# Kernel tuning notes

Measured on AMD Instinct MI355X. Metric: run time of the kernel, lower is better.

Reference implementation:

```python
import jax, jax.numpy as jnp
import numpy as np

STRIDE = 4
NUM_HEADS = 8


def _make_window(x, stride, nh):
    # (B,C,H,W) -> (B, nh, S, S, (H/S)*(W/S), C/nh)
    b, c, h, w = x.shape
    x = x.reshape(b, nh, c // nh, h // stride, stride, w // stride, stride)
    x = x.transpose(0, 1, 4, 6, 3, 5, 2)
    return x.reshape(b, nh, stride, stride, (h // stride) * (w // stride), c // nh)


def _demake_window(x, h, w):
    # (B, nh, S, S, L, dh) -> (B, nh*dh, H, W)
    b, nh, s, _, L, dh = x.shape
    x = x.reshape(b, nh, s, s, h // s, w // s, dh)
    x = x.transpose(0, 1, 6, 4, 2, 5, 3)
    return x.reshape(b, nh * dh, h, w)


def _proj(x, W, bias):
    # 1x1 conv == per-pixel GEMM: (B,C,H,W),(O,C) -> (B,O,H,W)
    return jnp.einsum('bchw,oc->bohw', x, W) + bias[None, :, None, None]


def setup_inputs() -> dict:
    key = jax.random.key(0)
    ks = jax.random.split(key, 12)
    B, C, H, W = 4, 256, 64, 64
    P, V, O = 256, 256, 256  # proj/value/out channels
    inp = {
        'fea_q': jax.random.normal(ks[0], (B, C, H, W), jnp.float32),
        'fea_k': jax.random.normal(ks[1], (B, C, H, W), jnp.float32),
        'fea_v': jax.random.normal(ks[2], (B, V, H, W), jnp.float32),
        'mask_q': (jax.random.uniform(ks[3], (B, 1, H, W)) > 0.5).astype(jnp.float32),
        'mask_k': (jax.random.uniform(ks[4], (B, 1, H, W)) > 0.5).astype(jnp.float32),
        'q_w': jax.random.normal(ks[5], (P, C), jnp.float32) * 0.02,
        'q_b': jnp.zeros((P,), jnp.float32),
        'k_w': jax.random.normal(ks[6], (P, C), jnp.float32) * 0.02,
        'k_b': jnp.zeros((P,), jnp.float32),
        'v_w': jax.random.normal(ks[7], (O, V), jnp.float32) * 0.02,
        'v_b': jnp.zeros((O,), jnp.float32),
    }
    return inp


def reference(fea_q, fea_k, fea_v, mask_q, mask_k, q_w, q_b, k_w, k_b, v_w, v_b):
    B, _, H, W = fea_q.shape
    head_dim = q_w.shape[0] // NUM_HEADS
    scaling = head_dim ** (-0.5)

    query = _make_window(_proj(fea_q, q_w, q_b), STRIDE, NUM_HEADS)
    key = _make_window(_proj(fea_k, k_w, k_b), STRIDE, NUM_HEADS)
    value = _make_window(_proj(fea_v, v_w, v_b), STRIDE, NUM_HEADS)

    # (B, nh, S, S, L, L)
    weights = jnp.matmul(query, jnp.swapaxes(key, -1, -2)) * scaling

    # mask attention (no-grad in original)
    mq = _make_window(jax.lax.stop_gradient(mask_q), STRIDE, 1)
    mk = _make_window(jax.lax.stop_gradient(mask_k), STRIDE, 1)
    mask_attn = jnp.matmul(mq, jnp.swapaxes(mk, -1, -2))  # (B,1,S,S,L,L)
    mask_sum = jnp.sum(mask_attn, axis=-1, keepdims=True)
    mask_attn = mask_attn + (mask_sum == 0).astype(jnp.float32)
    mask_attn = jnp.where(mask_attn == 0, -jnp.inf,
                          jnp.where(mask_attn == 1, 0.0, mask_attn))
    weights = weights + mask_attn

    weights = jax.nn.softmax(weights, axis=-1)  # dropout p=0 -> identity
    weights = weights * (1.0 - (mask_sum == 0).astype(jnp.float32))

    out = jnp.matmul(weights, value)  # (B, nh, S, S, L, dh)
    return _demake_window(out, H, W)
```

## Files before the change

### kernel.cpp

```cpp
#include <hip/hip_runtime.h>
#include <hip/hip_bf16.h>

#define NH 8
#define DH 32
#define LW 256
#define HW 4096
#define CIN 256

typedef float f32x4 __attribute__((ext_vector_type(4)));
typedef short s16x8 __attribute__((ext_vector_type(8)));
typedef short s16x4 __attribute__((ext_vector_type(4)));

#define AS1 __attribute__((address_space(1)))
#define AS3 __attribute__((address_space(3)))

__device__ __forceinline__ short f2bf(float f) {
  __hip_bfloat16 h = __float2bfloat16(f);
  short s; __builtin_memcpy(&s, &h, 2); return s;
}

__device__ __forceinline__ void gload_lds16(const void* g, void* l) {
  __builtin_amdgcn_global_load_lds((const AS1 void*)g, (AS3 void*)l, 16, 0, 0);
}

#define KOFF 4194304
#define VOFF 8388608
#define WTOFF 12582912

__global__ void wconv_kernel(const float* __restrict__ qw, const float* __restrict__ kw,
                             const float* __restrict__ vw, short* __restrict__ ws) {
  int blk = blockIdx.x;
  int t = blk >> 5, kb = blk & 31;
  const float* W = (t == 0) ? qw : ((t == 1) ? kw : vw);
  int o = threadIdx.x;
  f32x4 w0 = *(const f32x4*)(W + o * CIN + kb * 8);
  f32x4 w1 = *(const f32x4*)(W + o * CIN + kb * 8 + 4);
  s16x8 v;
#pragma unroll
  for (int j = 0; j < 4; ++j) { v[j] = f2bf(w0[j]); v[4 + j] = f2bf(w1[j]); }
  *(s16x8*)(ws + WTOFF + (blk * 256 + o) * 8) = v;
}

__global__ void __launch_bounds__(256, 3)
proj_kernel(const float* __restrict__ fq, const float* __restrict__ fk,
            const float* __restrict__ fv,
            const float* __restrict__ qb, const float* __restrict__ kb_,
            const float* __restrict__ vb,
            short* __restrict__ ws) {
  __shared__ s16x8 SMEM[2112];

  int bid = blockIdx.x;
  int orig = (bid & 7) * 96 + (bid >> 3);
  int t = orig >> 8;
  int r0 = orig & 255;
  int b = r0 >> 6;
  int pblk = r0 & 63;

  const float* fea = (t == 0) ? fq : ((t == 1) ? fk : fv);
  const float* Bv  = (t == 0) ? qb : ((t == 1) ? kb_ : vb);
  const short* Wt  = ws + WTOFF + t * 65536;

  int p0 = pblk * 64;
  int tid = threadIdx.x;
  int lane = tid & 63, wv = tid >> 6;
  int g = lane >> 4, li = lane & 15;

  const f32x4 fzero = {0.f, 0.f, 0.f, 0.f};
  f32x4 acc[4][4];
#pragma unroll
  for (int m = 0; m < 4; ++m)
#pragma unroll
    for (int n = 0; n < 4; ++n) acc[m][n] = fzero;

  const float* feab = fea + b * (CIN * HW);
  int wq = tid & 15;
  int jh = (tid >> 4) & 1;
  int coct = tid >> 5;

  f32x4 ldB[4];

#define LOAD_B(cs_) do { int c0_ = (cs_) * 64; _Pragma("unroll") \
  for (int j_ = 0; j_ < 4; ++j_) \
    ldB[j_] = *(const f32x4*)(feab + (c0_ + coct * 8 + jh * 4 + j_) * HW + p0 + wq * 4); } while (0)

#define WRITE_B(buf_) do { _Pragma("unroll") \
  for (int pp_ = 0; pp_ < 4; ++pp_) { s16x4 v_; _Pragma("unroll") \
    for (int j_ = 0; j_ < 4; ++j_) v_[j_] = f2bf(ldB[j_][pp_]); \
    int w_ = wq * 4 + pp_; int wsw_ = w_ ^ ((w_ >> 3) & 7); \
    *(s16x4*)((short*)SMEM + ((buf_) * 512 + coct * 64 + wsw_) * 8 + jh * 4) = v_; } } while (0)

  LOAD_B(0);
  WRITE_B(0);
  __syncthreads();

#pragma unroll
  for (int cs = 0; cs < 4; ++cs) {
    if (cs < 3) LOAD_B(cs + 1);
    s16x8 aF[2][4];
#pragma unroll
    for (int kk = 0; kk < 2; ++kk)
#pragma unroll
      for (int m = 0; m < 4; ++m)
        aF[kk][m] = *(const s16x8*)(Wt + ((cs * 8 + kk * 4 + g) * 256 + wv * 64 + m * 16 + li) * 8);
#pragma unroll
    for (int kk = 0; kk < 2; ++kk) {
#pragma unroll
      for (int n = 0; n < 4; ++n) {
        int w = n * 16 + li;
        int wsw = w ^ ((w >> 3) & 7);
        s16x8 bb = SMEM[(cs & 1) * 512 + (kk * 4 + g) * 64 + wsw];
#pragma unroll
        for (int m = 0; m < 4; ++m)
          acc[m][n] = __builtin_amdgcn_mfma_f32_16x16x32_bf16(aF[kk][m], bb, acc[m][n], 0, 0, 0);
      }
    }
    if (cs < 3) {
      WRITE_B((cs + 1) & 1);
      __syncthreads();
    }
  }
#undef LOAD_B
#undef WRITE_B

  float bias_r[4][4];
#pragma unroll
  for (int m = 0; m < 4; ++m) {
    f32x4 b4 = *(const f32x4*)(Bv + wv * 64 + m * 16 + g * 4);
#pragma unroll
    for (int rr = 0; rr < 4; ++rr) bias_r[m][rr] = b4[rr];
  }

  __syncthreads();
  short* Tr = (short*)SMEM;
#pragma unroll
  for (int m = 0; m < 4; ++m) {
    int ob = wv * 64 + m * 16 + g * 4;
#pragma unroll
    for (int n = 0; n < 4; ++n) {
      int w = n * 16 + li;
      s16x4 v;
#pragma unroll
      for (int rr = 0; rr < 4; ++rr) v[rr] = f2bf(acc[m][n][rr] + bias_r[m][rr]);
      *(s16x4*)(Tr + w * 264 + ob) = v;
    }
  }
  __syncthreads();

  int s1 = pblk & 3, h0 = pblk >> 2;
  if (t != 2) {
    short* dst = ws + (t == 0 ? 0 : KOFF);
#pragma unroll
    for (int it = 0; it < 8; ++it) {
      int o_oct = it * 4 + (tid >> 6);
      int w = tid & 63;
      s16x8 v = *(const s16x8*)(Tr + w * 264 + o_oct * 8);
      int o = o_oct * 8;
      int nh = o >> 5, kb = (o & 31) >> 3;
      int s2 = w & 3, w0 = w >> 2;
      int l = h0 * 16 + w0;
      int winbase = (b * NH + nh) * 16 + s1 * 4 + s2;
      *(s16x8*)(dst + winbase * 8192 + (kb * 256 + l) * 8) = v;
    }
  } else {
#pragma unroll
    for (int it = 0; it < 8; ++it) {
      int d = tid;
      int s2 = it & 3, w0h = it >> 2;
      int l_oct = h0 * 2 + w0h;
      s16x8 v;
#pragma unroll
      for (int k = 0; k < 8; ++k) {
        int w = (w0h * 8 + k) * 4 + s2;
        v[k] = Tr[w * 264 + d];
      }
      int dh = d & 31;
      int nh2 = d >> 5;
      int winbase = (b * NH + nh2) * 16 + s1 * 4 + s2;
      int idx = l_oct * 256 + (dh >> 4) * 128 + (dh & 15) * 8;
      *(s16x8*)(ws + VOFF + winbase * 8192 + idx) = v;
    }
  }
}

__global__ void __launch_bounds__(512, 4)
attn_kernel(const short* __restrict__ ws, const float* __restrict__ mq,
            const float* __restrict__ mk, float* __restrict__ out) {
  __shared__ s16x8 KsV[1024];
  __shared__ s16x8 PsV[1024];
  __shared__ float amaskS[256];
  __shared__ float mqS[256];
  __shared__ float facS[256];
  __shared__ int anyS[4];

  int bid = blockIdx.x;
  int orig = (bid & 7) * 64 + (bid >> 3);
  int s2 = orig & 3, s1 = (orig >> 2) & 3, nh = (orig >> 4) & 7, b = orig >> 7;
  int wwin = s1 * 4 + s2;
  int tid = threadIdx.x;
  int lane = tid & 63, wv = tid >> 6, g = lane >> 4, li = lane & 15;

  int winbase = (b * NH + nh) * 16 + wwin;
  const short* qt = ws + winbase * 8192;
  const short* kt = ws + KOFF + winbase * 8192;
  const short* vt = ws + VOFF + winbase * 8192;

#pragma unroll
  for (int i = 0; i < 2; ++i) {
    int seg = i * 8 + wv;
    gload_lds16(kt + (seg * 64 + lane) * 8, &KsV[seg * 64]);
  }

  if (tid < 256) {
    int l = tid;
    int h = (l >> 4) * 4 + s1, w = (l & 15) * 4 + s2;
    float mkv = mk[b * HW + h * 64 + w];
    amaskS[l] = (mkv > 0.5f) ? 0.0f : -1e30f;
    unsigned long long bal = __ballot(mkv > 0.5f);
    if (lane == 0) anyS[wv] = (bal != 0ULL) ? 1 : 0;
    mqS[l] = mq[b * HW + h * 64 + w];
  }

  int lq0 = wv * 32;
  s16x8 qa[2];
#pragma unroll
  for (int m = 0; m < 2; ++m)
    qa[m] = *(const s16x8*)(qt + (g * 256 + lq0 + m * 16 + li) * 8);

  __syncthreads();
  int anyk = anyS[0] | anyS[1] | anyS[2] | anyS[3];

  const f32x4 fzero = {0.f, 0.f, 0.f, 0.f};
  f32x4 of[2][2];
#pragma unroll
  for (int m = 0; m < 2; ++m) { of[m][0] = fzero; of[m][1] = fzero; }
  float rs[8];
#pragma unroll
  for (int i = 0; i < 8; ++i) rs[i] = 0.0f;

  const float C = 0.17677669529663689f * 1.4426950408889634f;

#pragma unroll
  for (int lkb = 0; lkb < 4; ++lkb) {
    f32x4 sa[2][4];
#pragma unroll
    for (int n = 0; n < 4; ++n) {
      s16x8 kf = KsV[g * 256 + lkb * 64 + n * 16 + li];
#pragma unroll
      for (int m = 0; m < 2; ++m)
        sa[m][n] = __builtin_amdgcn_mfma_f32_16x16x32_bf16(qa[m], kf, fzero, 0, 0, 0);
    }
#pragma unroll
    for (int ks = 0; ks < 2; ++ks) {
#pragma unroll
      for (int n2 = 0; n2 < 2; ++n2) {
        int n = ks * 2 + n2;
        float am = amaskS[lkb * 64 + n * 16 + li];
#pragma unroll
        for (int m = 0; m < 2; ++m) {
#pragma unroll
          for (int rr = 0; rr < 4; ++rr) {
            float pval = exp2f(sa[m][n][rr] * C + am);
            rs[m * 4 + rr] += pval;
            int row = m * 16 + g * 4 + rr;
            int cl = n * 16 + li;
            int kbh = (cl >> 3) & 3;
            short* ps = (short*)&PsV[wv * 128 + kbh * 32 + row];
            ps[cl & 7] = f2bf(pval);
          }
        }
      }
      int kg = lkb * 2 + ks;
      s16x8 pb[2];
#pragma unroll
      for (int n = 0; n < 2; ++n) pb[n] = PsV[wv * 128 + g * 32 + n * 16 + li];
#pragma unroll
      for (int m2 = 0; m2 < 2; ++m2) {
        s16x8 va = *(const s16x8*)(vt + (kg * 4 + g) * 256 + m2 * 128 + li * 8);
#pragma unroll
        for (int n = 0; n < 2; ++n)
          of[m2][n] = __builtin_amdgcn_mfma_f32_16x16x32_bf16(va, pb[n], of[m2][n], 0, 0, 0);
      }
    }
  }

#pragma unroll
  for (int i = 0; i < 8; ++i) {
    float v = rs[i];
    v += __shfl_xor(v, 1);
    v += __shfl_xor(v, 2);
    v += __shfl_xor(v, 4);
    v += __shfl_xor(v, 8);
    rs[i] = v;
  }
  if (li == 0) {
#pragma unroll
    for (int m = 0; m < 2; ++m)
#pragma unroll
      for (int rr = 0; rr < 4; ++rr) {
        int row = m * 16 + g * 4 + rr;
        float sum = rs[m * 4 + rr];
        facS[wv * 32 + row] = (anyk && mqS[wv * 32 + row] > 0.5f) ? (1.0f / sum) : 0.0f;
      }
  }

#pragma unroll
  for (int m2 = 0; m2 < 2; ++m2) {
#pragma unroll
    for (int n = 0; n < 2; ++n) {
      int l = wv * 32 + n * 16;
      float fac = facS[l + li];
      int h = (l >> 4) * 4 + s1;
      int w = li * 4 + s2;
#pragma unroll
      for (int rr = 0; rr < 4; ++rr) {
        int o = nh * 32 + m2 * 16 + g * 4 + rr;
        out[((b * 256 + o) * 64 + h) * 64 + w] = of[m2][n][rr] * fac;
      }
    }
  }
}

extern "C" void kernel_launch(void* const* d_in, const int* in_sizes, int n_in,
                              void* d_out, int out_size, void* d_ws, size_t ws_size,
                              hipStream_t stream) {
  const float* fq = (const float*)d_in[0];
  const float* fk = (const float*)d_in[1];
  const float* fv = (const float*)d_in[2];
  const float* mq = (const float*)d_in[3];
  const float* mk = (const float*)d_in[4];
  const float* qw = (const float*)d_in[5];
  const float* qb = (const float*)d_in[6];
  const float* kw = (const float*)d_in[7];
  const float* kb = (const float*)d_in[8];
  const float* vw = (const float*)d_in[9];
  const float* vb = (const float*)d_in[10];
  short* ws = (short*)d_ws;

  wconv_kernel<<<96, 256, 0, stream>>>(qw, kw, vw, ws);
  proj_kernel<<<768, 256, 0, stream>>>(fq, fk, fv, qb, kb, vb, ws);
  attn_kernel<<<512, 512, 0, stream>>>(ws, mq, mk, (float*)d_out);
}
```

Measured before the change: 48.71 us.

## Fuse projection and windowed attention into one kernel per window-head

Merges the separate projection kernel and attention kernel into one kernel in which each block projects the Q, K and V tiles for its own (batch, window, head) directly into LDS and then runs attention on them. This removes the bf16 Q/K/V round trip through global memory and one kernel launch. In exchange, each block re-reads the full 256-channel input features for its window's pixels with strided scalar fp32 loads, and those loads are repeated across the 8 heads. Block size also drops from 512 to 256 threads, with each wave handling more rows.

```diff
diff --git a/kernel.cpp b/kernel.cpp
--- a/kernel.cpp
+++ b/kernel.cpp
@@ -3,29 +3,17 @@
 
 #define NH 8
 #define DH 32
-#define LW 256
 #define HW 4096
 #define CIN 256
 
 typedef float f32x4 __attribute__((ext_vector_type(4)));
 typedef short s16x8 __attribute__((ext_vector_type(8)));
-typedef short s16x4 __attribute__((ext_vector_type(4)));
-
-#define AS1 __attribute__((address_space(1)))
-#define AS3 __attribute__((address_space(3)))
 
 __device__ __forceinline__ short f2bf(float f) {
   __hip_bfloat16 h = __float2bfloat16(f);
   short s; __builtin_memcpy(&s, &h, 2); return s;
 }
 
-__device__ __forceinline__ void gload_lds16(const void* g, void* l) {
-  __builtin_amdgcn_global_load_lds((const AS1 void*)g, (AS3 void*)l, 16, 0, 0);
-}
-
-#define KOFF 4194304
-#define VOFF 8388608
-#define WTOFF 12582912
 
 __global__ void wconv_kernel(const float* __restrict__ qw, const float* __restrict__ kw,
                              const float* __restrict__ vw, short* __restrict__ ws) {
@@ -38,155 +26,17 @@
   s16x8 v;
 #pragma unroll
   for (int j = 0; j < 4; ++j) { v[j] = f2bf(w0[j]); v[4 + j] = f2bf(w1[j]); }
-  *(s16x8*)(ws + WTOFF + (blk * 256 + o) * 8) = v;
-}
-
-__global__ void __launch_bounds__(256, 3)
-proj_kernel(const float* __restrict__ fq, const float* __restrict__ fk,
-            const float* __restrict__ fv,
-            const float* __restrict__ qb, const float* __restrict__ kb_,
-            const float* __restrict__ vb,
-            short* __restrict__ ws) {
-  __shared__ s16x8 SMEM[2112];
-
-  int bid = blockIdx.x;
-  int orig = (bid & 7) * 96 + (bid >> 3);
-  int t = orig >> 8;
-  int r0 = orig & 255;
-  int b = r0 >> 6;
-  int pblk = r0 & 63;
-
-  const float* fea = (t == 0) ? fq : ((t == 1) ? fk : fv);
-  const float* Bv  = (t == 0) ? qb : ((t == 1) ? kb_ : vb);
-  const short* Wt  = ws + WTOFF + t * 65536;
-
-  int p0 = pblk * 64;
-  int tid = threadIdx.x;
-  int lane = tid & 63, wv = tid >> 6;
-  int g = lane >> 4, li = lane & 15;
-
-  const f32x4 fzero = {0.f, 0.f, 0.f, 0.f};
-  f32x4 acc[4][4];
-#pragma unroll
-  for (int m = 0; m < 4; ++m)
-#pragma unroll
-    for (int n = 0; n < 4; ++n) acc[m][n] = fzero;
-
-  const float* feab = fea + b * (CIN * HW);
-  int wq = tid & 15;
-  int jh = (tid >> 4) & 1;
-  int coct = tid >> 5;
-
-  f32x4 ldB[4];
-
-#define LOAD_B(cs_) do { int c0_ = (cs_) * 64; _Pragma("unroll") \
-  for (int j_ = 0; j_ < 4; ++j_) \
-    ldB[j_] = *(const f32x4*)(feab + (c0_ + coct * 8 + jh * 4 + j_) * HW + p0 + wq * 4); } while (0)
-
-#define WRITE_B(buf_) do { _Pragma("unroll") \
-  for (int pp_ = 0; pp_ < 4; ++pp_) { s16x4 v_; _Pragma("unroll") \
-    for (int j_ = 0; j_ < 4; ++j_) v_[j_] = f2bf(ldB[j_][pp_]); \
-    int w_ = wq * 4 + pp_; int wsw_ = w_ ^ ((w_ >> 3) & 7); \
-    *(s16x4*)((short*)SMEM + ((buf_) * 512 + coct * 64 + wsw_) * 8 + jh * 4) = v_; } } while (0)
-
-  LOAD_B(0);
-  WRITE_B(0);
-  __syncthreads();
-
-#pragma unroll
-  for (int cs = 0; cs < 4; ++cs) {
-    if (cs < 3) LOAD_B(cs + 1);
-    s16x8 aF[2][4];
-#pragma unroll
-    for (int kk = 0; kk < 2; ++kk)
-#pragma unroll
-      for (int m = 0; m < 4; ++m)
-        aF[kk][m] = *(const s16x8*)(Wt + ((cs * 8 + kk * 4 + g) * 256 + wv * 64 + m * 16 + li) * 8);
-#pragma unroll
-    for (int kk = 0; kk < 2; ++kk) {
-#pragma unroll
-      for (int n = 0; n < 4; ++n) {
-        int w = n * 16 + li;
-        int wsw = w ^ ((w >> 3) & 7);
-        s16x8 bb = SMEM[(cs & 1) * 512 + (kk * 4 + g) * 64 + wsw];
-#pragma unroll
-        for (int m = 0; m < 4; ++m)
-          acc[m][n] = __builtin_amdgcn_mfma_f32_16x16x32_bf16(aF[kk][m], bb, acc[m][n], 0, 0, 0);
-      }
-    }
-    if (cs < 3) {
-      WRITE_B((cs + 1) & 1);
-      __syncthreads();
-    }
-  }
-#undef LOAD_B
-#undef WRITE_B
-
-  float bias_r[4][4];
-#pragma unroll
-  for (int m = 0; m < 4; ++m) {
-    f32x4 b4 = *(const f32x4*)(Bv + wv * 64 + m * 16 + g * 4);
-#pragma unroll
-    for (int rr = 0; rr < 4; ++rr) bias_r[m][rr] = b4[rr];
-  }
-
-  __syncthreads();
-  short* Tr = (short*)SMEM;
-#pragma unroll
-  for (int m = 0; m < 4; ++m) {
-    int ob = wv * 64 + m * 16 + g * 4;
-#pragma unroll
-    for (int n = 0; n < 4; ++n) {
-      int w = n * 16 + li;
-      s16x4 v;
-#pragma unroll
-      for (int rr = 0; rr < 4; ++rr) v[rr] = f2bf(acc[m][n][rr] + bias_r[m][rr]);
-      *(s16x4*)(Tr + w * 264 + ob) = v;
-    }
-  }
-  __syncthreads();
-
-  int s1 = pblk & 3, h0 = pblk >> 2;
-  if (t != 2) {
-    short* dst = ws + (t == 0 ? 0 : KOFF);
-#pragma unroll
-    for (int it = 0; it < 8; ++it) {
-      int o_oct = it * 4 + (tid >> 6);
-      int w = tid & 63;
-      s16x8 v = *(const s16x8*)(Tr + w * 264 + o_oct * 8);
-      int o = o_oct * 8;
-      int nh = o >> 5, kb = (o & 31) >> 3;
-      int s2 = w & 3, w0 = w >> 2;
-      int l = h0 * 16 + w0;
-      int winbase = (b * NH + nh) * 16 + s1 * 4 + s2;
-      *(s16x8*)(dst + winbase * 8192 + (kb * 256 + l) * 8) = v;
-    }
-  } else {
-#pragma unroll
-    for (int it = 0; it < 8; ++it) {
-      int d = tid;
-      int s2 = it & 3, w0h = it >> 2;
-      int l_oct = h0 * 2 + w0h;
-      s16x8 v;
-#pragma unroll
-      for (int k = 0; k < 8; ++k) {
-        int w = (w0h * 8 + k) * 4 + s2;
-        v[k] = Tr[w * 264 + d];
-      }
-      int dh = d & 31;
-      int nh2 = d >> 5;
-      int winbase = (b * NH + nh2) * 16 + s1 * 4 + s2;
-      int idx = l_oct * 256 + (dh >> 4) * 128 + (dh & 15) * 8;
-      *(s16x8*)(ws + VOFF + winbase * 8192 + idx) = v;
-    }
-  }
-}
-
-__global__ void __launch_bounds__(512, 4)
-attn_kernel(const short* __restrict__ ws, const float* __restrict__ mq,
-            const float* __restrict__ mk, float* __restrict__ out) {
-  __shared__ s16x8 KsV[1024];
-  __shared__ s16x8 PsV[1024];
+  *(s16x8*)(ws + (blk * 256 + o) * 8) = v;
+}
+
+__global__ void __launch_bounds__(256, 2)
+fused_kernel(const float* __restrict__ fq, const float* __restrict__ fk,
+             const float* __restrict__ fv,
+             const float* __restrict__ mq, const float* __restrict__ mk,
+             const float* __restrict__ qb, const float* __restrict__ kb_,
+             const float* __restrict__ vb,
+             const short* __restrict__ ws, float* __restrict__ out) {
+  __shared__ s16x8 IMG[4096];
   __shared__ float amaskS[256];
   __shared__ float mqS[256];
   __shared__ float facS[256];
@@ -194,23 +44,12 @@
 
   int bid = blockIdx.x;
   int orig = (bid & 7) * 64 + (bid >> 3);
-  int s2 = orig & 3, s1 = (orig >> 2) & 3, nh = (orig >> 4) & 7, b = orig >> 7;
-  int wwin = s1 * 4 + s2;
+  int nh = orig & 7, s2 = (orig >> 3) & 3, s1 = (orig >> 5) & 3, b = orig >> 7;
   int tid = threadIdx.x;
   int lane = tid & 63, wv = tid >> 6, g = lane >> 4, li = lane & 15;
-
-  int winbase = (b * NH + nh) * 16 + wwin;
-  const short* qt = ws + winbase * 8192;
-  const short* kt = ws + KOFF + winbase * 8192;
-  const short* vt = ws + VOFF + winbase * 8192;
-
-#pragma unroll
-  for (int i = 0; i < 2; ++i) {
-    int seg = i * 8 + wv;
-    gload_lds16(kt + (seg * 64 + lane) * 8, &KsV[seg * 64]);
-  }
-
-  if (tid < 256) {
+  int wl0 = wv * 64;
+
+  {
     int l = tid;
     int h = (l >> 4) * 4 + s1, w = (l & 15) * 4 + s2;
     float mkv = mk[b * HW + h * 64 + w];
@@ -220,33 +59,94 @@
     mqS[l] = mq[b * HW + h * 64 + w];
   }
 
-  int lq0 = wv * 32;
-  s16x8 qa[2];
-#pragma unroll
-  for (int m = 0; m < 2; ++m)
-    qa[m] = *(const s16x8*)(qt + (g * 256 + lq0 + m * 16 + li) * 8);
-
+  int hoff = ((tid >> 4) * 4 + s1) * 64 + (tid & 15) * 4 + s2;
+
+  const f32x4 fzero = {0.f, 0.f, 0.f, 0.f};
+#pragma unroll
+  for (int t = 0; t < 3; ++t) {
+    const float* feab = ((t == 0) ? fq : (t == 1) ? fk : fv) + b * (CIN * HW);
+    const float* Bv = (t == 0) ? qb : (t == 1) ? kb_ : vb;
+    const short* WtT = ws + t * 65536;
+
+    f32x4 acc[4][2];
+#pragma unroll
+    for (int m = 0; m < 4; ++m) { acc[m][0] = fzero; acc[m][1] = fzero; }
+
+#pragma unroll
+    for (int cc = 0; cc < 8; ++cc) {
+      __syncthreads();
+#pragma unroll
+      for (int i = 0; i < 4; ++i) {
+        s16x8 v;
+#pragma unroll
+        for (int j = 0; j < 8; ++j) {
+          int c = cc * 32 + i * 8 + j;
+          v[j] = f2bf(feab[c * HW + hoff]);
+        }
+        IMG[3072 + i * 256 + tid] = v;
+      }
+      __syncthreads();
+      s16x8 aF[4];
+#pragma unroll
+      for (int m = 0; m < 4; ++m)
+        aF[m] = IMG[3072 + g * 256 + wl0 + m * 16 + li];
+#pragma unroll
+      for (int n2 = 0; n2 < 2; ++n2) {
+        s16x8 bW = *(const s16x8*)(WtT + ((cc * 4 + g) * 256 + nh * 32 + n2 * 16 + li) * 8);
+#pragma unroll
+        for (int m = 0; m < 4; ++m)
+          acc[m][n2] = __builtin_amdgcn_mfma_f32_16x16x32_bf16(aF[m], bW, acc[m][n2], 0, 0, 0);
+      }
+    }
+    float bias0 = Bv[nh * 32 + li];
+    float bias1 = Bv[nh * 32 + 16 + li];
+#pragma unroll
+    for (int m = 0; m < 4; ++m) {
+#pragma unroll
+      for (int n2 = 0; n2 < 2; ++n2) {
+#pragma unroll
+        for (int rr = 0; rr < 4; ++rr) {
+          float val = acc[m][n2][rr] + (n2 ? bias1 : bias0);
+          int l = wl0 + m * 16 + g * 4 + rr;
+          int d = n2 * 16 + li;
+          if (t < 2) {
+            short* im = (short*)&IMG[t * 1024];
+            im[((d >> 3) * 256 + l) * 8 + (d & 7)] = f2bf(val);
+          } else {
+            short* im = (short*)&IMG[2048];
+            im[(l >> 3) * 256 + (d >> 4) * 128 + (d & 15) * 8 + (l & 7)] = f2bf(val);
+          }
+        }
+      }
+    }
+  }
   __syncthreads();
   int anyk = anyS[0] | anyS[1] | anyS[2] | anyS[3];
 
-  const f32x4 fzero = {0.f, 0.f, 0.f, 0.f};
-  f32x4 of[2][2];
-#pragma unroll
-  for (int m = 0; m < 2; ++m) { of[m][0] = fzero; of[m][1] = fzero; }
-  float rs[8];
-#pragma unroll
-  for (int i = 0; i < 8; ++i) rs[i] = 0.0f;
+  s16x8 qa[4];
+#pragma unroll
+  for (int m = 0; m < 4; ++m)
+    qa[m] = IMG[g * 256 + wl0 + m * 16 + li];
+
+  f32x4 of[2][4];
+#pragma unroll
+  for (int m2 = 0; m2 < 2; ++m2)
+#pragma unroll
+    for (int n = 0; n < 4; ++n) of[m2][n] = fzero;
+  float rs[16];
+#pragma unroll
+  for (int i = 0; i < 16; ++i) rs[i] = 0.0f;
 
   const float C = 0.17677669529663689f * 1.4426950408889634f;
 
 #pragma unroll
   for (int lkb = 0; lkb < 4; ++lkb) {
-    f32x4 sa[2][4];
+    f32x4 sa[4][4];
 #pragma unroll
     for (int n = 0; n < 4; ++n) {
-      s16x8 kf = KsV[g * 256 + lkb * 64 + n * 16 + li];
-#pragma unroll
-      for (int m = 0; m < 2; ++m)
+      s16x8 kf = IMG[1024 + g * 256 + lkb * 64 + n * 16 + li];
+#pragma unroll
+      for (int m = 0; m < 4; ++m)
         sa[m][n] = __builtin_amdgcn_mfma_f32_16x16x32_bf16(qa[m], kf, fzero, 0, 0, 0);
     }
 #pragma unroll
@@ -256,7 +156,7 @@
         int n = ks * 2 + n2;
         float am = amaskS[lkb * 64 + n * 16 + li];
 #pragma unroll
-        for (int m = 0; m < 2; ++m) {
+        for (int m = 0; m < 4; ++m) {
 #pragma unroll
           for (int rr = 0; rr < 4; ++rr) {
             float pval = exp2f(sa[m][n][rr] * C + am);
@@ -264,27 +164,28 @@
             int row = m * 16 + g * 4 + rr;
             int cl = n * 16 + li;
             int kbh = (cl >> 3) & 3;
-            short* ps = (short*)&PsV[wv * 128 + kbh * 32 + row];
+            short* ps = (short*)&IMG[3072 + wv * 256 + kbh * 64 + row];
             ps[cl & 7] = f2bf(pval);
           }
         }
       }
       int kg = lkb * 2 + ks;
-      s16x8 pb[2];
-#pragma unroll
-      for (int n = 0; n < 2; ++n) pb[n] = PsV[wv * 128 + g * 32 + n * 16 + li];
+      s16x8 pb[4];
+#pragma unroll
+      for (int n = 0; n < 4; ++n)
+        pb[n] = IMG[3072 + wv * 256 + g * 64 + n * 16 + li];
 #pragma unroll
       for (int m2 = 0; m2 < 2; ++m2) {
-        s16x8 va = *(const s16x8*)(vt + (kg * 4 + g) * 256 + m2 * 128 + li * 8);
-#pragma unroll
-        for (int n = 0; n < 2; ++n)
+        s16x8 va = *(const s16x8*)((short*)&IMG[2048] + (kg * 4 + g) * 256 + m2 * 128 + li * 8);
+#pragma unroll
+        for (int n = 0; n < 4; ++n)
           of[m2][n] = __builtin_amdgcn_mfma_f32_16x16x32_bf16(va, pb[n], of[m2][n], 0, 0, 0);
       }
     }
   }
 
 #pragma unroll
-  for (int i = 0; i < 8; ++i) {
+  for (int i = 0; i < 16; ++i) {
     float v = rs[i];
     v += __shfl_xor(v, 1);
     v += __shfl_xor(v, 2);
@@ -294,22 +195,22 @@
   }
   if (li == 0) {
 #pragma unroll
-    for (int m = 0; m < 2; ++m)
+    for (int m = 0; m < 4; ++m)
 #pragma unroll
       for (int rr = 0; rr < 4; ++rr) {
-        int row = m * 16 + g * 4 + rr;
+        int row = wl0 + m * 16 + g * 4 + rr;
         float sum = rs[m * 4 + rr];
-        facS[wv * 32 + row] = (anyk && mqS[wv * 32 + row] > 0.5f) ? (1.0f / sum) : 0.0f;
+        facS[row] = (anyk && mqS[row] > 0.5f) ? (1.0f / sum) : 0.0f;
       }
   }
 
 #pragma unroll
   for (int m2 = 0; m2 < 2; ++m2) {
 #pragma unroll
-    for (int n = 0; n < 2; ++n) {
-      int l = wv * 32 + n * 16;
-      float fac = facS[l + li];
-      int h = (l >> 4) * 4 + s1;
+    for (int n = 0; n < 4; ++n) {
+      int lloc = wl0 + n * 16;
+      float fac = facS[lloc + li];
+      int h = (lloc >> 4) * 4 + s1;
       int w = li * 4 + s2;
 #pragma unroll
       for (int rr = 0; rr < 4; ++rr) {
@@ -337,6 +238,5 @@
   short* ws = (short*)d_ws;
 
   wconv_kernel<<<96, 256, 0, stream>>>(qw, kw, vw, ws);
-  proj_kernel<<<768, 256, 0, stream>>>(fq, fk, fv, qb, kb, vb, ws);
-  attn_kernel<<<512, 512, 0, stream>>>(ws, mq, mk, (float*)d_out);
-}
+  fused_kernel<<<512, 256, 0, stream>>>(fq, fk, fv, mq, mk, qb, kb, vb, ws, (float*)d_out);
+}
```

Measured after the change: 128.4 us. 2.64x slower.
